# Kernel tuning notes

Measured on AMD Instinct MI355X. Metric: run time of the kernel, lower is better.

## Reference

```python
import jax, jax.numpy as jnp
import numpy as np

N, E, D, H, L, T = 50000, 200000, 128, 64, 2, 4
SIB_ID = 1
EPS = 1e-6


def _log_map_zero(x, c):
    # x: [N, D+1] on hyperboloid of curvature c; returns [N, D] tangent at origin.
    sqrt_c = jnp.sqrt(c)
    x0 = jnp.clip(sqrt_c * x[..., 0], 1.0 + 1e-7, None)
    dist = jnp.arccosh(x0) / sqrt_c                      # [N]
    sp = x[..., 1:]                                      # [N, D]
    nrm = jnp.maximum(jnp.linalg.norm(sp, axis=-1), EPS)
    return sp * (dist / nrm)[..., None]


def _exp_map_zero(v, c):
    # v: [N, D] tangent at origin; returns [N, D+1] on hyperboloid.
    sqrt_c = jnp.sqrt(c)
    nrm = jnp.maximum(jnp.linalg.norm(v, axis=-1), EPS)  # [N]
    th = sqrt_c * nrm
    x0 = jnp.cosh(th) / sqrt_c
    sp = v * (jnp.sinh(th) / (sqrt_c * nrm))[..., None]
    return jnp.concatenate([x0[..., None], sp], axis=-1)


def setup_inputs() -> dict:
    key = jax.random.key(0)
    ks = jax.random.split(key, 12)
    v0 = 0.1 * jax.random.normal(ks[0], (N, D), dtype=jnp.float32)
    x_hyp = _exp_map_zero(v0, 1.0)
    edge_index = jax.random.randint(ks[1], (2, E), 0, N, dtype=jnp.int32)
    edge_types = jax.random.randint(ks[2], (E,), 0, T, dtype=jnp.int32)
    edge_weights = jax.random.uniform(ks[3], (E,), dtype=jnp.float32) + 0.1
    s_lin = 1.0 / np.sqrt(D)
    s_w1 = 1.0 / np.sqrt(3 * D)
    s_w2 = 1.0 / np.sqrt(H)
    return {
        "x_hyp": x_hyp,
        "edge_index": edge_index,
        "edge_types": edge_types,
        "edge_weights": edge_weights,
        "lin_w": s_lin * jax.random.normal(ks[4], (L, D, D), dtype=jnp.float32),
        "lin_b": jnp.zeros((L, D), dtype=jnp.float32),
        "ln_g": jnp.ones((L, D), dtype=jnp.float32),
        "ln_b": jnp.zeros((L, D), dtype=jnp.float32),
        "edge_emb": 0.02 * jax.random.normal(ks[5], (L, T, D), dtype=jnp.float32),
        "attn_w1": s_w1 * jax.random.normal(ks[6], (L, 3 * D, H), dtype=jnp.float32),
        "attn_b1": jnp.zeros((L, H), dtype=jnp.float32),
        "attn_w2": s_w2 * jax.random.normal(ks[7], (L, H, 1), dtype=jnp.float32),
        "attn_b2": jnp.zeros((L, 1), dtype=jnp.float32),
        "sibling_boost": jnp.full((L,), 0.15, dtype=jnp.float32),
        "curvature": jnp.ones((L,), dtype=jnp.float32),
    }


def _layer(x_hyp, edge_index, edge_types, edge_weights,
           lin_w, lin_b, ln_g, ln_b, emb, w1, b1, w2, b2, sib, curv):
    n = x_hyp.shape[0]
    # curvature is read via .item() in the original -> detached constant
    c = jax.lax.stop_gradient(jnp.clip(curv, 0.1, 10.0))
    x_tan = _log_map_zero(x_hyp, c)                      # [N, D]
    x_lin = x_tan @ lin_w.T + lin_b                      # [N, D]
    src, dst = edge_index[0], edge_index[1]              # PyG: x_j=src, x_i=dst
    x_i = x_lin[dst]                                     # [E, D]
    x_j = x_lin[src]                                     # [E, D]
    e_emb = emb[edge_types]                              # [E, D]
    attn_in = jnp.concatenate([x_i, x_j, e_emb], axis=-1)  # [E, 3D]
    h = jax.nn.silu(attn_in @ w1 + b1)                   # [E, H]
    score = (h @ w2 + b2)[..., 0]                        # [E]
    score = score + jnp.log(jnp.clip(edge_weights, EPS, None))
    score = score + (edge_types == SIB_ID).astype(score.dtype) * sib
    # segment softmax over destination nodes
    seg_max = jax.ops.segment_max(score, dst, num_segments=n)
    ex = jnp.exp(score - seg_max[dst])
    seg_sum = jax.ops.segment_sum(ex, dst, num_segments=n)
    alpha = ex / (seg_sum[dst] + 1e-16)                  # [E]
    msg = (x_j + e_emb) * (alpha * edge_weights)[:, None]  # [E, D]
    x_agg = jax.ops.segment_sum(msg, dst, num_segments=n)  # [N, D]
    x_out = x_tan + x_agg                                # dropout is identity in eval
    mu = jnp.mean(x_out, axis=-1, keepdims=True)
    var = jnp.var(x_out, axis=-1, keepdims=True)
    x_out = (x_out - mu) * jax.lax.rsqrt(var + 1e-5) * ln_g + ln_b
    return _exp_map_zero(x_out, c)


def reference(x_hyp, edge_index, edge_types, edge_weights, lin_w, lin_b,
              ln_g, ln_b, edge_emb, attn_w1, attn_b1, attn_w2, attn_b2,
              sibling_boost, curvature):
    for i in range(lin_w.shape[0]):
        x_hyp = _layer(x_hyp, edge_index, edge_types, edge_weights,
                       lin_w[i], lin_b[i], ln_g[i], ln_b[i], edge_emb[i],
                       attn_w1[i], attn_b1[i], attn_w2[i], attn_b2[i],
                       sibling_boost[i], curvature[i])
    return x_hyp
```

## Files before the change

### kernel.cpp

```cpp
#include <hip/hip_runtime.h>
#include <hip/hip_bf16.h>
#include <math.h>

#define WAVE 64
#define KMAX 32

typedef __attribute__((ext_vector_type(8))) short bf16x8;
typedef __attribute__((ext_vector_type(4))) float f32x4;

__device__ __forceinline__ unsigned short f2b(float f) {
    unsigned u = __float_as_uint(f);
    unsigned r = (u + 0x7FFFu + ((u >> 16) & 1u)) >> 16;
    return (unsigned short)r;
}
__device__ __forceinline__ float b2f(unsigned short u) {
    return __uint_as_float(((unsigned)u) << 16);
}
__device__ __forceinline__ float frcp(float x)   { return __builtin_amdgcn_rcpf(x); }
__device__ __forceinline__ float frsq(float x)   { return __builtin_amdgcn_rsqf(x); }
__device__ __forceinline__ float fsqrt2(float x) { return __builtin_amdgcn_sqrtf(x); }
__device__ __forceinline__ float silu(float x)   { return x * frcp(1.f + __expf(-x)); }
__device__ __forceinline__ float facosh(float x) { return __logf(x + fsqrt2(x * x - 1.f)); }

__global__ __launch_bounds__(256) void k_prep_hist(
    const float* __restrict__ lin_w, const float* __restrict__ w1,
    const float* __restrict__ b1, const float* __restrict__ emb,
    const int* __restrict__ ei, const int* __restrict__ et,
    const float* __restrict__ ew, const float* __restrict__ xh,
    const float* __restrict__ curv,
    unsigned short* __restrict__ lw_bf, unsigned short* __restrict__ Wt_bf,
    float* __restrict__ ae, int* __restrict__ deg, int2* __restrict__ epack,
    unsigned short* __restrict__ xtan_bf, int E, int N, int PB, int ECH)
{
    int bid = blockIdx.x, tid = threadIdx.x;
    if (bid < PB) {
        int l = bid / 129, bx = bid % 129;
        const float* lwl = lin_w + (size_t)l * 16384;
        const float* w1l = w1 + (size_t)l * 384 * 64;
        if (bx < 64) {
            int idx = bx * 256 + tid;
            lw_bf[l * 16384 + idx] = f2b(lwl[idx]);
        } else if (bx < 128) {
            int idx = (bx - 64) * 256 + tid;
            int o = idx >> 7, i = idx & 127;
            float v = (o < 64) ? w1l[i * 64 + o] : w1l[(128 + i) * 64 + (o - 64)];
            Wt_bf[l * 16384 + idx] = f2b(v);
        } else {
            int t = tid >> 6, h = tid & 63;
            float s = b1[l * 64 + h];
            #pragma unroll 8
            for (int i = 0; i < 128; ++i)
                s += emb[l * 512 + t * 128 + i] * w1l[(256 + i) * 64 + h];
            ae[l * 256 + tid] = s;
        }
    } else if (bid < PB + ECH) {
        int e = (bid - PB) * 256 + tid;
        if (e < E) {
            int dst = ei[E + e];
            int rank = atomicAdd(&deg[dst], 1);
            if (rank < KMAX) {
                int2 r;
                r.x = ei[e] | (et[e] << 24);
                r.y = __float_as_int(ew[e]);
                epack[(size_t)dst * KMAX + rank] = r;
            }
        }
    } else {
        int wid = (bid - PB - ECH) * 4 + (tid >> 6);
        int lane = tid & 63;
        if (wid >= N) return;
        float c = fminf(fmaxf(curv[0], 0.1f), 10.f);
        float sqc = fsqrt2(c);
        const float* row = xh + (size_t)wid * 129;
        float x0 = row[0];
        float s0 = row[1 + lane];
        float s1 = row[65 + lane];
        float n2 = s0 * s0 + s1 * s1;
        #pragma unroll
        for (int off = 32; off > 0; off >>= 1) n2 += __shfl_xor(n2, off, WAVE);
        float nrm = fmaxf(fsqrt2(n2), 1e-6f);
        float x0c = fmaxf(sqc * x0, 1.f + 1e-7f);
        float f = facosh(x0c) * frcp(sqc) * frcp(nrm);
        unsigned short* ob = xtan_bf + (size_t)wid * 128;
        ob[lane] = f2b(s0 * f);
        ob[64 + lane] = f2b(s1 * f);
    }
}

__global__ __launch_bounds__(256) void k_A(
    const unsigned short* __restrict__ xtan_bf,
    const unsigned short* __restrict__ LW, const unsigned short* __restrict__ WT,
    const float* __restrict__ bias, unsigned short* __restrict__ xlin,
    unsigned short* __restrict__ acat, int M)
{
    __shared__ unsigned short xs[64 * 136];
    int wave = threadIdx.x >> 6;
    int lane = threadIdx.x & 63;
    int quad = lane >> 4;
    int l16  = lane & 15;
    int m0w = blockIdx.x * 64 + wave * 16;
    int row = m0w + l16;
    int rowc = row < M ? row : M - 1;

    bf16x8 a[4];
    #pragma unroll
    for (int kk = 0; kk < 4; ++kk)
        a[kk] = *(const bf16x8*)&xtan_bf[(size_t)rowc * 128 + kk * 32 + quad * 8];

    f32x4 acc[8];
    #pragma unroll
    for (int nt = 0; nt < 8; ++nt) acc[nt] = (f32x4){0.f, 0.f, 0.f, 0.f};
    #pragma unroll
    for (int kk = 0; kk < 4; ++kk) {
        #pragma unroll
        for (int nt = 0; nt < 8; ++nt) {
            bf16x8 b = *(const bf16x8*)&LW[(size_t)(nt * 16 + l16) * 128 + kk * 32 + quad * 8];
            acc[nt] = __builtin_amdgcn_mfma_f32_16x16x32_bf16(a[kk], b, acc[nt], 0, 0, 0);
        }
    }
    #pragma unroll
    for (int nt = 0; nt < 8; ++nt) {
        float bv = bias[nt * 16 + l16];
        #pragma unroll
        for (int r = 0; r < 4; ++r) {
            int lrow = wave * 16 + quad * 4 + r;
            xs[lrow * 136 + nt * 16 + l16] = f2b(acc[nt][r] + bv);
        }
    }
    __syncthreads();

    bf16x8 a2[4];
    int lr = wave * 16 + l16;
    #pragma unroll
    for (int kk = 0; kk < 4; ++kk) {
        a2[kk] = *(const bf16x8*)&xs[lr * 136 + kk * 32 + quad * 8];
        if (row < M)
            *(bf16x8*)&xlin[(size_t)row * 128 + kk * 32 + quad * 8] = a2[kk];
    }

    f32x4 acc2[8];
    #pragma unroll
    for (int nt = 0; nt < 8; ++nt) acc2[nt] = (f32x4){0.f, 0.f, 0.f, 0.f};
    #pragma unroll
    for (int kk = 0; kk < 4; ++kk) {
        #pragma unroll
        for (int nt = 0; nt < 8; ++nt) {
            bf16x8 b = *(const bf16x8*)&WT[(size_t)(nt * 16 + l16) * 128 + kk * 32 + quad * 8];
            acc2[nt] = __builtin_amdgcn_mfma_f32_16x16x32_bf16(a2[kk], b, acc2[nt], 0, 0, 0);
        }
    }
    #pragma unroll
    for (int nt = 0; nt < 8; ++nt) {
        #pragma unroll
        for (int r = 0; r < 4; ++r) {
            int rr = m0w + quad * 4 + r;
            if (rr < M) acat[(size_t)rr * 128 + nt * 16 + l16] = f2b(acc2[nt][r]);
        }
    }
}

__global__ __launch_bounds__(256) void k_B(
    const int* __restrict__ deg, const int2* __restrict__ epack,
    const unsigned short* __restrict__ acat, const unsigned short* __restrict__ xlin,
    unsigned short* __restrict__ xtan_bf, const float* __restrict__ ae,
    const float* __restrict__ emb, const float* __restrict__ w2,
    const float* __restrict__ b2, const float* __restrict__ sib,
    const float* __restrict__ g, const float* __restrict__ b,
    const float* __restrict__ curv, const float* __restrict__ curv_n,
    int last, float* __restrict__ out, int N)
{
    int tid = threadIdx.x;
    int lane = tid & 63;
    int quad = lane >> 4;
    int l16  = lane & 15;
    int gw = (blockIdx.x * 256 + tid) >> 6;
    int wid = gw * 4 + quad;
    bool nv = wid < N;
    int widc = nv ? wid : N - 1;

    float c = fminf(fmaxf(curv[0], 0.1f), 10.f);
    float sqc = fsqrt2(c);
    float rsqc = frcp(sqc);
    int dg = deg[widc];
    dg = dg < KMAX ? dg : KMAX;
    int p0 = widc * KMAX;
    int p1 = nv ? p0 + dg : p0;

    ushort4 adu = *(const ushort4*)&acat[(size_t)widc * 128 + 4 * l16];
    float ad0 = b2f(adu.x), ad1 = b2f(adu.y), ad2 = b2f(adu.z), ad3 = b2f(adu.w);
    float4 w2v = *(const float4*)&w2[4 * l16];
    float b2v = b2[0], sibv = sib[0];

    float acc[8];
    #pragma unroll
    for (int j = 0; j < 8; ++j) acc[j] = 0.f;
    float S = 0.f;
    float4 St = make_float4(0.f, 0.f, 0.f, 0.f);

    for (int j = 0; ; ++j) {
        int p = p0 + j;
        bool ev = p < p1;
        if (!__any(ev)) break;
        int2 r = epack[ev ? p : 0];
        int src = r.x & 0xFFFFFF;
        int t = ((unsigned)r.x) >> 24;
        float w = __int_as_float(r.y);

        ushort4 asu = *(const ushort4*)&acat[(size_t)src * 128 + 64 + 4 * l16];
        float4 av = *(const float4*)&ae[t * 64 + 4 * l16];
        float d = silu(ad0 + b2f(asu.x) + av.x) * w2v.x
                + silu(ad1 + b2f(asu.y) + av.y) * w2v.y
                + silu(ad2 + b2f(asu.z) + av.z) * w2v.z
                + silu(ad3 + b2f(asu.w) + av.w) * w2v.w;
        #pragma unroll
        for (int m = 1; m < 16; m <<= 1) d += __shfl_xor(d, m, WAVE);
        float s = d + b2v + __logf(fmaxf(w, 1e-6f));
        if (t == 1) s += sibv;
        float exv = ev ? __expf(s) : 0.f;
        S += exv;
        float cf = exv * w;

        bf16x8 xu = *(const bf16x8*)&xlin[(size_t)src * 128 + 8 * l16];
        #pragma unroll
        for (int k = 0; k < 8; ++k)
            acc[k] += b2f((unsigned short)xu[k]) * cf;
        St.x += (t == 0) ? cf : 0.f;
        St.y += (t == 1) ? cf : 0.f;
        St.z += (t == 2) ? cf : 0.f;
        St.w += (t == 3) ? cf : 0.f;
    }

    #pragma unroll
    for (int tt = 0; tt < 4; ++tt) {
        float stv = (tt == 0) ? St.x : (tt == 1) ? St.y : (tt == 2) ? St.z : St.w;
        float4 em0 = *(const float4*)&emb[tt * 128 + 8 * l16];
        float4 em1 = *(const float4*)&emb[tt * 128 + 8 * l16 + 4];
        acc[0] += em0.x * stv; acc[1] += em0.y * stv;
        acc[2] += em0.z * stv; acc[3] += em0.w * stv;
        acc[4] += em1.x * stv; acc[5] += em1.y * stv;
        acc[6] += em1.z * stv; acc[7] += em1.w * stv;
    }

    float inv = frcp(S + 1e-16f);
    bf16x8 xtu = *(const bf16x8*)&xtan_bf[(size_t)widc * 128 + 8 * l16];
    float y[8];
    #pragma unroll
    for (int j = 0; j < 8; ++j)
        y[j] = b2f((unsigned short)xtu[j]) + acc[j] * inv;

    float sum = 0.f, sq = 0.f;
    #pragma unroll
    for (int j = 0; j < 8; ++j) { sum += y[j]; sq += y[j] * y[j]; }
    #pragma unroll
    for (int m = 1; m < 16; m <<= 1) {
        sum += __shfl_xor(sum, m, WAVE);
        sq  += __shfl_xor(sq, m, WAVE);
    }
    float mu = sum * (1.f / 128.f);
    float var = sq * (1.f / 128.f) - mu * mu;
    float invs = frsq(var + 1e-5f);
    float4 g0 = *(const float4*)&g[8 * l16];
    float4 g1 = *(const float4*)&g[8 * l16 + 4];
    float4 bb0 = *(const float4*)&b[8 * l16];
    float4 bb1 = *(const float4*)&b[8 * l16 + 4];
    y[0] = (y[0] - mu) * invs * g0.x + bb0.x;
    y[1] = (y[1] - mu) * invs * g0.y + bb0.y;
    y[2] = (y[2] - mu) * invs * g0.z + bb0.z;
    y[3] = (y[3] - mu) * invs * g0.w + bb0.w;
    y[4] = (y[4] - mu) * invs * g1.x + bb1.x;
    y[5] = (y[5] - mu) * invs * g1.y + bb1.y;
    y[6] = (y[6] - mu) * invs * g1.z + bb1.z;
    y[7] = (y[7] - mu) * invs * g1.w + bb1.w;

    float nrm2 = 0.f;
    #pragma unroll
    for (int j = 0; j < 8; ++j) nrm2 += y[j] * y[j];
    #pragma unroll
    for (int m = 1; m < 16; m <<= 1) nrm2 += __shfl_xor(nrm2, m, WAVE);
    float nrm = fmaxf(fsqrt2(nrm2), 1e-6f);
    float th = sqc * nrm;
    float e = __expf(th);
    float einv = frcp(e);
    float ch = 0.5f * (e + einv);
    float sh = 0.5f * (e - einv);
    float sc = sh * frcp(sqc * nrm);

    if (last) {
        if (nv) {
            float* o = out + (size_t)wid * 129;
            if (l16 == 0) o[0] = ch * rsqc;
            #pragma unroll
            for (int j = 0; j < 8; ++j) o[1 + 8 * l16 + j] = y[j] * sc;
        }
    } else {
        float x0 = ch * rsqc;
        float c2 = fminf(fmaxf(curv_n[0], 0.1f), 10.f);
        float sqc2 = fsqrt2(c2);
        float x0c = fmaxf(sqc2 * x0, 1.f + 1e-7f);
        float dist = facosh(x0c) * frcp(sqc2);
        float nsp = fmaxf(sh * rsqc, 1e-6f);
        float sf = sc * dist * frcp(nsp);
        if (nv) {
            bf16x8 o8;
            #pragma unroll
            for (int j = 0; j < 8; ++j) o8[j] = (short)f2b(y[j] * sf);
            *(bf16x8*)&xtan_bf[(size_t)wid * 128 + 8 * l16] = o8;
        }
    }
}

extern "C" void kernel_launch(void* const* d_in, const int* in_sizes, int n_in,
                              void* d_out, int out_size, void* d_ws, size_t ws_size,
                              hipStream_t stream) {
    const float* x_hyp = (const float*)d_in[0];
    const int*   ei    = (const int*)d_in[1];
    const int*   et    = (const int*)d_in[2];
    const float* ew    = (const float*)d_in[3];
    const float* lin_w = (const float*)d_in[4];
    const float* lin_b = (const float*)d_in[5];
    const float* ln_g  = (const float*)d_in[6];
    const float* ln_b  = (const float*)d_in[7];
    const float* emb   = (const float*)d_in[8];
    const float* w1    = (const float*)d_in[9];
    const float* b1    = (const float*)d_in[10];
    const float* w2    = (const float*)d_in[11];
    const float* b2    = (const float*)d_in[12];
    const float* sib   = (const float*)d_in[13];
    const float* curv  = (const float*)d_in[14];
    float* out = (float*)d_out;
    float* ws  = (float*)d_ws;

    const int N = in_sizes[0] / 129;
    const int E = in_sizes[2];
    const int L = in_sizes[4] / (128 * 128);
    const int ECH = (E + 255) / 256;
    const int ATL = (N + 63) / 64;
    const int NLG = (N + 3) / 4;
    const int PB = L * 129;

    unsigned short* xtan_bf = (unsigned short*)ws;
    unsigned short* xlin_bf = xtan_bf + (size_t)N * 128;
    unsigned short* acat_bf = xlin_bf + (size_t)N * 128;
    int2* epack = (int2*)(acat_bf + (size_t)N * 128);
    unsigned short* lw_bf = (unsigned short*)(epack + (size_t)N * KMAX);
    unsigned short* Wt_bf = lw_bf + (size_t)L * 16384;
    float* ae   = (float*)(Wt_bf + (size_t)L * 16384);
    int* deg    = (int*)(ae + (size_t)L * 256);

    hipMemsetAsync(deg, 0, (size_t)N * sizeof(int), stream);
    k_prep_hist<<<PB + ECH + NLG, 256, 0, stream>>>(
        lin_w, w1, b1, emb, ei, et, ew, x_hyp, curv,
        lw_bf, Wt_bf, ae, deg, epack, xtan_bf, E, N, PB, ECH);

    for (int l = 0; l < L; ++l) {
        k_A<<<ATL, 256, 0, stream>>>(
            xtan_bf, lw_bf + (size_t)l * 16384, Wt_bf + (size_t)l * 16384,
            lin_b + (size_t)l * 128, xlin_bf, acat_bf, N);
        k_B<<<(N + 15) / 16, 256, 0, stream>>>(
            deg, epack, acat_bf, xlin_bf, xtan_bf,
            ae + (size_t)l * 256, emb + (size_t)l * 512,
            w2 + (size_t)l * 64, b2 + l, sib + l,
            ln_g + (size_t)l * 128, ln_b + (size_t)l * 128,
            curv + l, curv + (l + 1 < L ? l + 1 : l),
            l == L - 1 ? 1 : 0, out, N);
    }
}
```

Baseline: 247.0 us.

## Fuse per-layer dual GEMM into log-map and aggregation kernels

Drops the separate k_A launches. The next layer's two bf16 MFMA GEMMs now run at the tail of k_B, and the first layer's run inside a new k_main that also does the edge histogram and the initial log-map. xlin/acat buffers are double-buffered so k_B can read the current layer's values while writing the next layer's, and the hipMemset of deg is replaced by zeroing inside k_pre. This saves kernel launches and a global round trip of xtan into the GEMM, at the cost of 16-row tiles with shared LDS staging and reloading the weight matrices for every block.

After: 222.5 us. 9.9% less time.

```diff
diff --git a/kernel.cpp b/kernel.cpp
--- a/kernel.cpp
+++ b/kernel.cpp
@@ -1,5 +1,4 @@
 #include <hip/hip_runtime.h>
-#include <hip/hip_bf16.h>
 #include <math.h>
 
 #define WAVE 64
@@ -22,15 +21,86 @@
 __device__ __forceinline__ float silu(float x)   { return x * frcp(1.f + __expf(-x)); }
 __device__ __forceinline__ float facosh(float x) { return __logf(x + fsqrt2(x * x - 1.f)); }
 
-__global__ __launch_bounds__(256) void k_prep_hist(
+__device__ __forceinline__ void dual_gemm_16(
+    unsigned short* sm,
+    const unsigned short* __restrict__ LW, const unsigned short* __restrict__ WT,
+    const float* __restrict__ bias,
+    unsigned short* __restrict__ xlin, unsigned short* __restrict__ acat,
+    int base, int N, int tid)
+{
+    int wave = tid >> 6;
+    int lane = tid & 63;
+    int quad = lane >> 4;
+    int l16  = lane & 15;
+    int nloc = tid >> 4;
+
+    __syncthreads();
+
+    bf16x8 a[4];
+    #pragma unroll
+    for (int kk = 0; kk < 4; ++kk)
+        a[kk] = *(const bf16x8*)&sm[l16 * 136 + kk * 32 + quad * 8];
+
+    f32x4 acc[2];
+    acc[0] = (f32x4){0.f, 0.f, 0.f, 0.f};
+    acc[1] = (f32x4){0.f, 0.f, 0.f, 0.f};
+    #pragma unroll
+    for (int kk = 0; kk < 4; ++kk) {
+        #pragma unroll
+        for (int t = 0; t < 2; ++t) {
+            int nt = wave * 2 + t;
+            bf16x8 b = *(const bf16x8*)&LW[(size_t)(nt * 16 + l16) * 128 + kk * 32 + quad * 8];
+            acc[t] = __builtin_amdgcn_mfma_f32_16x16x32_bf16(a[kk], b, acc[t], 0, 0, 0);
+        }
+    }
+    __syncthreads();
+    #pragma unroll
+    for (int t = 0; t < 2; ++t) {
+        int nt = wave * 2 + t;
+        float bv = bias[nt * 16 + l16];
+        #pragma unroll
+        for (int r = 0; r < 4; ++r)
+            sm[(quad * 4 + r) * 136 + nt * 16 + l16] = f2b(acc[t][r] + bv);
+    }
+    __syncthreads();
+
+    bf16x8 a2[4];
+    #pragma unroll
+    for (int kk = 0; kk < 4; ++kk)
+        a2[kk] = *(const bf16x8*)&sm[l16 * 136 + kk * 32 + quad * 8];
+    int node = base + nloc;
+    if (node < N)
+        *(bf16x8*)&xlin[(size_t)node * 128 + 8 * l16] =
+            *(const bf16x8*)&sm[nloc * 136 + 8 * l16];
+
+    f32x4 acc2[2];
+    acc2[0] = (f32x4){0.f, 0.f, 0.f, 0.f};
+    acc2[1] = (f32x4){0.f, 0.f, 0.f, 0.f};
+    #pragma unroll
+    for (int kk = 0; kk < 4; ++kk) {
+        #pragma unroll
+        for (int t = 0; t < 2; ++t) {
+            int nt = wave * 2 + t;
+            bf16x8 b = *(const bf16x8*)&WT[(size_t)(nt * 16 + l16) * 128 + kk * 32 + quad * 8];
+            acc2[t] = __builtin_amdgcn_mfma_f32_16x16x32_bf16(a2[kk], b, acc2[t], 0, 0, 0);
+        }
+    }
+    #pragma unroll
+    for (int t = 0; t < 2; ++t) {
+        int nt = wave * 2 + t;
+        #pragma unroll
+        for (int r = 0; r < 4; ++r) {
+            int rr = base + quad * 4 + r;
+            if (rr < N) acat[(size_t)rr * 128 + nt * 16 + l16] = f2b(acc2[t][r]);
+        }
+    }
+}
+
+__global__ __launch_bounds__(256) void k_pre(
     const float* __restrict__ lin_w, const float* __restrict__ w1,
     const float* __restrict__ b1, const float* __restrict__ emb,
-    const int* __restrict__ ei, const int* __restrict__ et,
-    const float* __restrict__ ew, const float* __restrict__ xh,
-    const float* __restrict__ curv,
     unsigned short* __restrict__ lw_bf, unsigned short* __restrict__ Wt_bf,
-    float* __restrict__ ae, int* __restrict__ deg, int2* __restrict__ epack,
-    unsigned short* __restrict__ xtan_bf, int E, int N, int PB, int ECH)
+    float* __restrict__ ae, int* __restrict__ deg, int N, int PB)
 {
     int bid = blockIdx.x, tid = threadIdx.x;
     if (bid < PB) {
@@ -53,8 +123,33 @@
                 s += emb[l * 512 + t * 128 + i] * w1l[(256 + i) * 64 + h];
             ae[l * 256 + tid] = s;
         }
-    } else if (bid < PB + ECH) {
-        int e = (bid - PB) * 256 + tid;
+    } else {
+        int i0 = ((bid - PB) * 256 + tid) * 4;
+        if (i0 + 3 < N) {
+            *(int4*)&deg[i0] = make_int4(0, 0, 0, 0);
+        } else {
+            #pragma unroll
+            for (int k2 = 0; k2 < 4; ++k2)
+                if (i0 + k2 < N) deg[i0 + k2] = 0;
+        }
+    }
+}
+
+__global__ __launch_bounds__(256) void k_main(
+    const int* __restrict__ ei, const int* __restrict__ et,
+    const float* __restrict__ ew, const float* __restrict__ xh,
+    const float* __restrict__ curv,
+    const unsigned short* __restrict__ LW, const unsigned short* __restrict__ WT,
+    const float* __restrict__ lb,
+    int* __restrict__ deg, int2* __restrict__ epack,
+    unsigned short* __restrict__ xtan_bf,
+    unsigned short* __restrict__ xlin, unsigned short* __restrict__ acat,
+    int E, int N, int ECH)
+{
+    __shared__ __align__(16) unsigned short sm[16 * 136];
+    int bid = blockIdx.x, tid = threadIdx.x;
+    if (bid < ECH) {
+        int e = bid * 256 + tid;
         if (e < E) {
             int dst = ei[E + e];
             int rank = atomicAdd(&deg[dst], 1);
@@ -65,98 +160,38 @@
                 epack[(size_t)dst * KMAX + rank] = r;
             }
         }
-    } else {
-        int wid = (bid - PB - ECH) * 4 + (tid >> 6);
-        int lane = tid & 63;
-        if (wid >= N) return;
-        float c = fminf(fmaxf(curv[0], 0.1f), 10.f);
-        float sqc = fsqrt2(c);
-        const float* row = xh + (size_t)wid * 129;
-        float x0 = row[0];
-        float s0 = row[1 + lane];
-        float s1 = row[65 + lane];
-        float n2 = s0 * s0 + s1 * s1;
-        #pragma unroll
-        for (int off = 32; off > 0; off >>= 1) n2 += __shfl_xor(n2, off, WAVE);
-        float nrm = fmaxf(fsqrt2(n2), 1e-6f);
-        float x0c = fmaxf(sqc * x0, 1.f + 1e-7f);
-        float f = facosh(x0c) * frcp(sqc) * frcp(nrm);
-        unsigned short* ob = xtan_bf + (size_t)wid * 128;
-        ob[lane] = f2b(s0 * f);
-        ob[64 + lane] = f2b(s1 * f);
-    }
-}
-
-__global__ __launch_bounds__(256) void k_A(
-    const unsigned short* __restrict__ xtan_bf,
-    const unsigned short* __restrict__ LW, const unsigned short* __restrict__ WT,
-    const float* __restrict__ bias, unsigned short* __restrict__ xlin,
-    unsigned short* __restrict__ acat, int M)
-{
-    __shared__ unsigned short xs[64 * 136];
-    int wave = threadIdx.x >> 6;
-    int lane = threadIdx.x & 63;
-    int quad = lane >> 4;
-    int l16  = lane & 15;
-    int m0w = blockIdx.x * 64 + wave * 16;
-    int row = m0w + l16;
-    int rowc = row < M ? row : M - 1;
-
-    bf16x8 a[4];
-    #pragma unroll
-    for (int kk = 0; kk < 4; ++kk)
-        a[kk] = *(const bf16x8*)&xtan_bf[(size_t)rowc * 128 + kk * 32 + quad * 8];
-
-    f32x4 acc[8];
-    #pragma unroll
-    for (int nt = 0; nt < 8; ++nt) acc[nt] = (f32x4){0.f, 0.f, 0.f, 0.f};
-    #pragma unroll
-    for (int kk = 0; kk < 4; ++kk) {
-        #pragma unroll
-        for (int nt = 0; nt < 8; ++nt) {
-            bf16x8 b = *(const bf16x8*)&LW[(size_t)(nt * 16 + l16) * 128 + kk * 32 + quad * 8];
-            acc[nt] = __builtin_amdgcn_mfma_f32_16x16x32_bf16(a[kk], b, acc[nt], 0, 0, 0);
-        }
-    }
-    #pragma unroll
-    for (int nt = 0; nt < 8; ++nt) {
-        float bv = bias[nt * 16 + l16];
-        #pragma unroll
-        for (int r = 0; r < 4; ++r) {
-            int lrow = wave * 16 + quad * 4 + r;
-            xs[lrow * 136 + nt * 16 + l16] = f2b(acc[nt][r] + bv);
-        }
-    }
-    __syncthreads();
-
-    bf16x8 a2[4];
-    int lr = wave * 16 + l16;
-    #pragma unroll
-    for (int kk = 0; kk < 4; ++kk) {
-        a2[kk] = *(const bf16x8*)&xs[lr * 136 + kk * 32 + quad * 8];
-        if (row < M)
-            *(bf16x8*)&xlin[(size_t)row * 128 + kk * 32 + quad * 8] = a2[kk];
-    }
-
-    f32x4 acc2[8];
-    #pragma unroll
-    for (int nt = 0; nt < 8; ++nt) acc2[nt] = (f32x4){0.f, 0.f, 0.f, 0.f};
-    #pragma unroll
-    for (int kk = 0; kk < 4; ++kk) {
-        #pragma unroll
-        for (int nt = 0; nt < 8; ++nt) {
-            bf16x8 b = *(const bf16x8*)&WT[(size_t)(nt * 16 + l16) * 128 + kk * 32 + quad * 8];
-            acc2[nt] = __builtin_amdgcn_mfma_f32_16x16x32_bf16(a2[kk], b, acc2[nt], 0, 0, 0);
-        }
-    }
-    #pragma unroll
-    for (int nt = 0; nt < 8; ++nt) {
-        #pragma unroll
-        for (int r = 0; r < 4; ++r) {
-            int rr = m0w + quad * 4 + r;
-            if (rr < M) acat[(size_t)rr * 128 + nt * 16 + l16] = f2b(acc2[nt][r]);
-        }
-    }
+        return;
+    }
+    int base = (bid - ECH) * 16;
+    int l16  = tid & 15;
+    int nloc = tid >> 4;
+    int node = base + nloc;
+    int nodec = node < N ? node : N - 1;
+
+    float c = fminf(fmaxf(curv[0], 0.1f), 10.f);
+    float sqc = fsqrt2(c);
+    const float* row = xh + (size_t)nodec * 129;
+    float x0 = row[0];
+    float v[8];
+    #pragma unroll
+    for (int j = 0; j < 8; ++j) v[j] = row[1 + 8 * l16 + j];
+    float n2 = 0.f;
+    #pragma unroll
+    for (int j = 0; j < 8; ++j) n2 += v[j] * v[j];
+    #pragma unroll
+    for (int m = 1; m < 16; m <<= 1) n2 += __shfl_xor(n2, m, WAVE);
+    float nrm = fmaxf(fsqrt2(n2), 1e-6f);
+    float x0c = fmaxf(sqc * x0, 1.f + 1e-7f);
+    float f = facosh(x0c) * frcp(sqc) * frcp(nrm);
+
+    bf16x8 o8;
+    #pragma unroll
+    for (int j = 0; j < 8; ++j) o8[j] = (short)f2b(v[j] * f);
+    if (node < N)
+        *(bf16x8*)&xtan_bf[(size_t)node * 128 + 8 * l16] = o8;
+    *(bf16x8*)&sm[nloc * 136 + 8 * l16] = o8;
+
+    dual_gemm_16(sm, LW, WT, lb, xlin, acat, base, N, tid);
 }
 
 __global__ __launch_bounds__(256) void k_B(
@@ -167,8 +202,12 @@
     const float* __restrict__ b2, const float* __restrict__ sib,
     const float* __restrict__ g, const float* __restrict__ b,
     const float* __restrict__ curv, const float* __restrict__ curv_n,
-    int last, float* __restrict__ out, int N)
+    int last, float* __restrict__ out, int N,
+    const unsigned short* __restrict__ LWn, const unsigned short* __restrict__ WTn,
+    const float* __restrict__ lbn,
+    unsigned short* __restrict__ xlin_o, unsigned short* __restrict__ acat_o)
 {
+    __shared__ __align__(16) unsigned short sm[16 * 136];
     int tid = threadIdx.x;
     int lane = tid & 63;
     int quad = lane >> 4;
@@ -300,12 +339,13 @@
         float dist = facosh(x0c) * frcp(sqc2);
         float nsp = fmaxf(sh * rsqc, 1e-6f);
         float sf = sc * dist * frcp(nsp);
-        if (nv) {
-            bf16x8 o8;
-            #pragma unroll
-            for (int j = 0; j < 8; ++j) o8[j] = (short)f2b(y[j] * sf);
+        bf16x8 o8;
+        #pragma unroll
+        for (int j = 0; j < 8; ++j) o8[j] = (short)f2b(y[j] * sf);
+        if (nv)
             *(bf16x8*)&xtan_bf[(size_t)wid * 128 + 8 * l16] = o8;
-        }
+        *(bf16x8*)&sm[(tid >> 4) * 136 + 8 * l16] = o8;
+        dual_gemm_16(sm, LWn, WTn, lbn, xlin_o, acat_o, blockIdx.x * 16, N, tid);
     }
 }
 
@@ -328,40 +368,47 @@
     const float* sib   = (const float*)d_in[13];
     const float* curv  = (const float*)d_in[14];
     float* out = (float*)d_out;
-    float* ws  = (float*)d_ws;
 
     const int N = in_sizes[0] / 129;
     const int E = in_sizes[2];
     const int L = in_sizes[4] / (128 * 128);
     const int ECH = (E + 255) / 256;
-    const int ATL = (N + 63) / 64;
-    const int NLG = (N + 3) / 4;
+    const int NB16 = (N + 15) / 16;
     const int PB = L * 129;
-
-    unsigned short* xtan_bf = (unsigned short*)ws;
-    unsigned short* xlin_bf = xtan_bf + (size_t)N * 128;
-    unsigned short* acat_bf = xlin_bf + (size_t)N * 128;
-    int2* epack = (int2*)(acat_bf + (size_t)N * 128);
+    const int ZB = (N + 1023) / 1024;
+
+    unsigned short* xtan_bf = (unsigned short*)d_ws;
+    unsigned short* xlin0 = xtan_bf + (size_t)N * 128;
+    unsigned short* acat0 = xlin0 + (size_t)N * 128;
+    unsigned short* xlin1 = acat0 + (size_t)N * 128;
+    unsigned short* acat1 = xlin1 + (size_t)N * 128;
+    int2* epack = (int2*)(acat1 + (size_t)N * 128);
     unsigned short* lw_bf = (unsigned short*)(epack + (size_t)N * KMAX);
     unsigned short* Wt_bf = lw_bf + (size_t)L * 16384;
     float* ae   = (float*)(Wt_bf + (size_t)L * 16384);
     int* deg    = (int*)(ae + (size_t)L * 256);
 
-    hipMemsetAsync(deg, 0, (size_t)N * sizeof(int), stream);
-    k_prep_hist<<<PB + ECH + NLG, 256, 0, stream>>>(
-        lin_w, w1, b1, emb, ei, et, ew, x_hyp, curv,
-        lw_bf, Wt_bf, ae, deg, epack, xtan_bf, E, N, PB, ECH);
+    k_pre<<<PB + ZB, 256, 0, stream>>>(lin_w, w1, b1, emb,
+                                       lw_bf, Wt_bf, ae, deg, N, PB);
+
+    k_main<<<ECH + NB16, 256, 0, stream>>>(
+        ei, et, ew, x_hyp, curv, lw_bf, Wt_bf, lin_b,
+        deg, epack, xtan_bf, xlin0, acat0, E, N, ECH);
 
     for (int l = 0; l < L; ++l) {
-        k_A<<<ATL, 256, 0, stream>>>(
-            xtan_bf, lw_bf + (size_t)l * 16384, Wt_bf + (size_t)l * 16384,
-            lin_b + (size_t)l * 128, xlin_bf, acat_bf, N);
-        k_B<<<(N + 15) / 16, 256, 0, stream>>>(
-            deg, epack, acat_bf, xlin_bf, xtan_bf,
+        int ln = (l + 1 < L) ? l + 1 : l;
+        unsigned short* xin = (l & 1) ? xlin1 : xlin0;
+        unsigned short* ain = (l & 1) ? acat1 : acat0;
+        unsigned short* xot = (l & 1) ? xlin0 : xlin1;
+        unsigned short* aot = (l & 1) ? acat0 : acat1;
+        k_B<<<NB16, 256, 0, stream>>>(
+            deg, epack, ain, xin, xtan_bf,
             ae + (size_t)l * 256, emb + (size_t)l * 512,
             w2 + (size_t)l * 64, b2 + l, sib + l,
             ln_g + (size_t)l * 128, ln_b + (size_t)l * 128,
-            curv + l, curv + (l + 1 < L ? l + 1 : l),
-            l == L - 1 ? 1 : 0, out, N);
-    }
-}
+            curv + l, curv + ln,
+            l == L - 1 ? 1 : 0, out, N,
+            lw_bf + (size_t)ln * 16384, Wt_bf + (size_t)ln * 16384,
+            lin_b + (size_t)ln * 128, xot, aot);
+    }
+}
```
